# Performance work log

Measured on AMD Instinct MI355X. Metric: run time of the kernel, lower is better.

## Reference

```python
import jax, jax.numpy as jnp
from jax import lax
import numpy as np

NUM_HEADS = 8
K_RATIO = 0.5
GN_EPS = 1e-6
CLAMP = 32.0          # fp32 branch of the torch code
FILL = -1e9           # fp32 masked-fill value
L2_EPS = 1e-12        # torch F.normalize eps


def setup_inputs() -> dict:
    key = jax.random.key(0)
    k1, k2, k3 = jax.random.split(key, 3)
    B, C, H, W = 1, 256, 64, 64
    x = jax.random.normal(k1, (B, C, H, W), dtype=jnp.float32)
    w_qkv = jax.random.normal(k2, (3 * C, C), dtype=jnp.float32) * 0.02  # 1x1 conv, no bias
    w_proj = jax.random.normal(k3, (C, C), dtype=jnp.float32) * 0.02     # 1x1 conv, no bias
    gamma = jnp.ones((C,), dtype=jnp.float32)   # GroupNorm affine
    beta = jnp.zeros((C,), dtype=jnp.float32)
    return {"x": x, "w_qkv": w_qkv, "w_proj": w_proj, "gamma": gamma, "beta": beta}


def _l2norm(t):
    n = jnp.sqrt(jnp.sum(t * t, axis=-1, keepdims=True))
    return t / jnp.maximum(n, L2_EPS)


def reference(x, w_qkv, w_proj, gamma, beta):
    B, C, H, W = x.shape
    N = H * W
    hd = C // NUM_HEADS
    scale = hd ** -0.5

    # qkv 1x1 conv -> [B, 3C, H, W] -> [B, 3, heads, hd, N]
    qkv = jnp.einsum('bchw,oc->bohw', x, w_qkv).reshape(B, 3, NUM_HEADS, hd, N)
    q = jnp.swapaxes(qkv[:, 0], -1, -2)  # [B, heads, N, hd]
    k = jnp.swapaxes(qkv[:, 1], -1, -2)
    v = jnp.swapaxes(qkv[:, 2], -1, -2)

    q = _l2norm(q)
    k = _l2norm(k)

    attn = jnp.einsum('bhnd,bhmd->bhnm', q, k) * scale  # [B, heads, N, N]
    attn = jnp.clip(attn, -CLAMP, CLAMP)

    k_num = max(int(N * K_RATIO), 1)
    if k_num < N:
        # keep only top-k per row; threshold at the k-th largest value
        # (equivalent to torch.topk + scatter mask for continuous-valued scores)
        kth = lax.top_k(attn, k_num)[0][..., -1:]
        attn = jnp.where(attn >= kth, attn, FILL)

    attn = jax.nn.softmax(attn, axis=-1)
    out = jnp.einsum('bhnm,bhmd->bhnd', attn, v)          # [B, heads, N, hd]
    out = jnp.swapaxes(out, -1, -2).reshape(B, C, H, W)   # transpose(2,3) + reshape

    out = jnp.einsum('bchw,oc->bohw', out, w_proj)        # proj 1x1 conv

    # GroupNorm(groups=min(32, C//4)=32, eps=1e-6) with affine
    G = min(32, C // 4)
    xg = out.reshape(B, G, -1)
    mean = jnp.mean(xg, axis=-1, keepdims=True)
    var = jnp.var(xg, axis=-1, keepdims=True)
    xg = (xg - mean) / jnp.sqrt(var + GN_EPS)
    out = xg.reshape(B, C, H, W) * gamma[None, :, None, None] + beta[None, :, None, None]
    return out
```

## Files before the change

kernel.cpp:

```cpp
#include <hip/hip_runtime.h>


#define NTOK 4096
#define HD 32
#define NHEADS 8
#define KSEL 2048
#define SCALE 0.17677669529663689f
#define LOG2C 7.73937f


__device__ __forceinline__ unsigned fkey(float f) {
  unsigned b = __float_as_uint(f);
  return (b & 0x80000000u) ? ~b : (b | 0x80000000u);
}
__device__ __forceinline__ float unfkey(unsigned k) {
  unsigned b = (k & 0x80000000u) ? (k ^ 0x80000000u) : ~k;
  return __uint_as_float(b);
}
__device__ __forceinline__ unsigned rfl_u(unsigned x) {
  return __builtin_amdgcn_readfirstlane(x);
}
__device__ __forceinline__ unsigned probe_rf(unsigned klo, unsigned khi,
                                             float xlo, float xhi,
                                             int clo, int chi) {
  float t = xlo + (xhi - xlo) * ((float)(clo - KSEL) / (float)(clo - chi));
  unsigned k = fkey(t);
  if (k <= klo) k = klo + 1u;
  if (k > khi) k = khi;
  return k;
}


template <bool SCATTER>
__global__ __launch_bounds__(256) void gemm_k256(
    const float* __restrict__ A, const float* __restrict__ B,
    float* __restrict__ C0, float* __restrict__ C1, float* __restrict__ C2) {
  __shared__ float Wt[64][17];
  __shared__ float Xt[16][64];

  const int tid = threadIdx.x;
  const int tx = tid & 15, ty = tid >> 4;
  const int o0 = blockIdx.y * 64, n0 = blockIdx.x * 64;

  const int wr = tid >> 2, wc = (tid & 3) << 2;
  const int xr = tid >> 4, xc = (tid & 15) << 2;

  float4 acc[4];
#pragma unroll
  for (int i = 0; i < 4; ++i) acc[i] = make_float4(0.f, 0.f, 0.f, 0.f);

  for (int k0 = 0; k0 < 256; k0 += 16) {
    float4 wv = *(const float4*)(A + (o0 + wr) * 256 + k0 + wc);
    float4 xv = *(const float4*)(B + (k0 + xr) * 4096 + n0 + xc);
    Wt[wr][wc + 0] = wv.x; Wt[wr][wc + 1] = wv.y;
    Wt[wr][wc + 2] = wv.z; Wt[wr][wc + 3] = wv.w;
    *(float4*)&Xt[xr][xc] = xv;
    __syncthreads();
#pragma unroll
    for (int kk = 0; kk < 16; ++kk) {
      float4 b = *(const float4*)&Xt[kk][tx << 2];
#pragma unroll
      for (int i = 0; i < 4; ++i) {
        float a = Wt[(ty << 2) + i][kk];
        acc[i].x += a * b.x; acc[i].y += a * b.y;
        acc[i].z += a * b.z; acc[i].w += a * b.w;
      }
    }
    __syncthreads();
  }

  if (SCATTER) {
#pragma unroll
    for (int i = 0; i < 4; ++i) {
      int o = o0 + (ty << 2) + i;
      int which = o >> 8, rem = o & 255;
      int h = rem >> 5, d = rem & 31;
      int n = n0 + (tx << 2);
      if (which == 1) {
        *(float4*)(C1 + h * (HD * NTOK) + d * NTOK + n) = acc[i];
      } else {
        float* dst = (which == 0) ? C0 : C2;
        int base = h * (NTOK * HD) + d;
        dst[base + (n + 0) * HD] = acc[i].x;
        dst[base + (n + 1) * HD] = acc[i].y;
        dst[base + (n + 2) * HD] = acc[i].z;
        dst[base + (n + 3) * HD] = acc[i].w;
      }
    }
  } else {
#pragma unroll
    for (int i = 0; i < 4; ++i) {
      int o = o0 + (ty << 2) + i;
      *(float4*)(C0 + o * 4096 + n0 + (tx << 2)) = acc[i];
    }
  }
}


__global__ __launch_bounds__(256) void l2norm_q(float* __restrict__ Q) {
  const int tid = threadIdx.x;
  const int p = blockIdx.x * 8 + (tid >> 5);
  const int d = tid & 31;
  const int idx = p * HD + d;
  float v = Q[idx];
  float ss = v * v;
#pragma unroll
  for (int m = 16; m >= 1; m >>= 1) ss += __shfl_xor(ss, m, 32);
  float nrm = sqrtf(ss);
  Q[idx] = v * SCALE / fmaxf(nrm, 1e-12f);
}


__global__ __launch_bounds__(256) void l2norm_kt(float* __restrict__ KT) {
  const int n = blockIdx.x * 256 + threadIdx.x;
  float* P = KT + blockIdx.y * (HD * NTOK) + n;
  float v[HD];
  float ss = 0.f;
#pragma unroll
  for (int d = 0; d < HD; ++d) {
    v[d] = P[d * NTOK];
    ss += v[d] * v[d];
  }
  float inv = 1.f / fmaxf(sqrtf(ss), 1e-12f);
#pragma unroll
  for (int d = 0; d < HD; ++d) P[d * NTOK] = v[d] * inv;
}


__global__ __launch_bounds__(256, 5) void attn_kernel(
    const float* __restrict__ Q, const float* __restrict__ KT,
    const float* __restrict__ V, float* __restrict__ AO) {
  __shared__ __align__(16) unsigned char wtsT[NTOK][4];
  __shared__ float qs[128];
  __shared__ float pvred[4 * 8 * 4 * 4];
  __shared__ unsigned ired[2][4][2];
  __shared__ unsigned dred[4][4];

  const int tid = threadIdx.x;
  const int wv = tid >> 6, lane = tid & 63;
  const int head = blockIdx.x & 7;
  const int n0 = (blockIdx.x >> 3) << 2;

  const float* Qh = Q + head * (NTOK * HD);
  const float* KTh = KT + head * (HD * NTOK);
  const float* Vh = V + head * (NTOK * HD);

  if (tid < 128) qs[tid] = Qh[n0 * HD + tid];
  __syncthreads();

  float kr[4][16];
#pragma unroll
  for (int r = 0; r < 4; ++r)
#pragma unroll
    for (int j = 0; j < 16; ++j) kr[r][j] = 0.f;

  const int cb = tid << 2;
  const float* kbase = KTh + cb;
#define QK8(r, q, a, b, j0)                                                  \
  kr[r][(j0) + 0] += (q) * (a).x; kr[r][(j0) + 1] += (q) * (a).y;            \
  kr[r][(j0) + 2] += (q) * (a).z; kr[r][(j0) + 3] += (q) * (a).w;            \
  kr[r][(j0) + 4] += (q) * (b).x; kr[r][(j0) + 5] += (q) * (b).y;            \
  kr[r][(j0) + 6] += (q) * (b).z; kr[r][(j0) + 7] += (q) * (b).w;
#pragma unroll 1
  for (int dg = 0; dg < 8; ++dg) {
#pragma unroll 1
    for (int dd = 0; dd < 4; ++dd) {
      const int d = (dg << 2) + dd;
      const float* kp = kbase + d * NTOK;
      const float4 a0 = *(const float4*)(kp);
      const float4 b0 = *(const float4*)(kp + 1024);
      const float4 a1 = *(const float4*)(kp + 2048);
      const float4 b1 = *(const float4*)(kp + 3072);
      const float q0 = qs[d];
      const float q1 = qs[HD + d];
      const float q2 = qs[2 * HD + d];
      const float q3 = qs[3 * HD + d];
      QK8(0, q0, a0, b0, 0) QK8(1, q1, a0, b0, 0)
      QK8(2, q2, a0, b0, 0) QK8(3, q3, a0, b0, 0)
      QK8(0, q0, a1, b1, 8) QK8(1, q1, a1, b1, 8)
      QK8(2, q2, a1, b1, 8) QK8(3, q3, a1, b1, 8)
    }
  }
#undef QK8

  unsigned klo0 = 0x417FFFFFu, khi0 = 0xBE800000u;
  unsigned klo1 = 0x417FFFFFu, khi1 = 0xBE800000u;
  unsigned klo2 = 0x417FFFFFu, khi2 = 0xBE800000u;
  unsigned klo3 = 0x417FFFFFu, khi3 = 0xBE800000u;
  float xlo0 = -0.25f, xhi0 = 0.25f, xlo1 = -0.25f, xhi1 = 0.25f;
  float xlo2 = -0.25f, xhi2 = 0.25f, xlo3 = -0.25f, xhi3 = 0.25f;
  int clo0 = NTOK, chi0 = 0, clo1 = NTOK, chi1 = 0;
  int clo2 = NTOK, chi2 = 0, clo3 = NTOK, chi3 = 0;
  bool dn0 = false, dn1 = false, dn2 = false, dn3 = false;
  int slot = 0;
#pragma unroll 1
  for (int it = 0; it < 40; ++it) {
    unsigned m0 = dn0 ? klo0
        : ((it < 8 && (khi0 - klo0) > 65536u)
               ? rfl_u(probe_rf(klo0, khi0, xlo0, xhi0, clo0, chi0))
               : klo0 + ((khi0 - klo0 + 1u) >> 1));
    unsigned m1 = dn1 ? klo1
        : ((it < 8 && (khi1 - klo1) > 65536u)
               ? rfl_u(probe_rf(klo1, khi1, xlo1, xhi1, clo1, chi1))
               : klo1 + ((khi1 - klo1 + 1u) >> 1));
    unsigned m2 = dn2 ? klo2
        : ((it < 8 && (khi2 - klo2) > 65536u)
               ? rfl_u(probe_rf(klo2, khi2, xlo2, xhi2, clo2, chi2))
               : klo2 + ((khi2 - klo2 + 1u) >> 1));
    unsigned m3 = dn3 ? klo3
        : ((it < 8 && (khi3 - klo3) > 65536u)
               ? rfl_u(probe_rf(klo3, khi3, xlo3, xhi3, clo3, chi3))
               : klo3 + ((khi3 - klo3 + 1u) >> 1));
    unsigned c0 = 0, c1 = 0, c2 = 0, c3 = 0;
    if (!dn0) {
      const float f0 = unfkey(m0);
#pragma unroll
      for (int j = 0; j < 16; ++j) c0 += __popcll(__ballot(kr[0][j] >= f0));
    }
    if (!dn1) {
      const float f1 = unfkey(m1);
#pragma unroll
      for (int j = 0; j < 16; ++j) c1 += __popcll(__ballot(kr[1][j] >= f1));
    }
    if (!dn2) {
      const float f2 = unfkey(m2);
#pragma unroll
      for (int j = 0; j < 16; ++j) c2 += __popcll(__ballot(kr[2][j] >= f2));
    }
    if (!dn3) {
      const float f3 = unfkey(m3);
#pragma unroll
      for (int j = 0; j < 16; ++j) c3 += __popcll(__ballot(kr[3][j] >= f3));
    }
    if (lane == 0) {
      ired[slot][wv][0] = c0 | (c1 << 16);
      ired[slot][wv][1] = c2 | (c3 << 16);
    }
    __syncthreads();
    unsigned a01 = rfl_u(ired[slot][0][0] + ired[slot][1][0] +
                         ired[slot][2][0] + ired[slot][3][0]);
    unsigned a23 = rfl_u(ired[slot][0][1] + ired[slot][1][1] +
                         ired[slot][2][1] + ired[slot][3][1]);
    slot ^= 1;
    int C0 = (int)(a01 & 0xFFFFu), C1 = (int)(a01 >> 16);
    int C2 = (int)(a23 & 0xFFFFu), C3 = (int)(a23 >> 16);
#define BUPD(C, klo, khi, xlo, xhi, clo, chi, dn, mk)                        \
    if (!dn) {                                                               \
      if (C == KSEL) { klo = mk; dn = true; }                                \
      else if (C > KSEL) { klo = mk; xlo = unfkey(mk); clo = C; }            \
      else { khi = mk - 1u; xhi = unfkey(mk); chi = C; }                     \
      if (klo >= khi) dn = true;                                             \
    }
    BUPD(C0, klo0, khi0, xlo0, xhi0, clo0, chi0, dn0, m0)
    BUPD(C1, klo1, khi1, xlo1, xhi1, clo1, chi1, dn1, m1)
    BUPD(C2, klo2, khi2, xlo2, xhi2, clo2, chi2, dn2, m2)
    BUPD(C3, klo3, khi3, xlo3, xhi3, clo3, chi3, dn3, m3)
#undef BUPD
    if (dn0 && dn1 && dn2 && dn3) break;
  }
  const float tf0 = unfkey(klo0), tf1 = unfkey(klo1);
  const float tf2 = unfkey(klo2), tf3 = unfkey(klo3);

  unsigned id0 = 0, id1 = 0, id2 = 0, id3 = 0;
#pragma unroll
  for (int g = 0; g < 4; ++g) {
    unsigned pk[4];
#pragma unroll
    for (int t = 0; t < 4; ++t) {
      const int j = (g << 2) + t;
      float s0 = kr[0][j], s1 = kr[1][j], s2 = kr[2][j], s3 = kr[3][j];
      unsigned u0 = (s0 >= tf0) ? (unsigned)rintf(exp2f(__builtin_fmaf(s0, 1.44269504f, LOG2C))) : 0u;
      unsigned u1 = (s1 >= tf1) ? (unsigned)rintf(exp2f(__builtin_fmaf(s1, 1.44269504f, LOG2C))) : 0u;
      unsigned u2 = (s2 >= tf2) ? (unsigned)rintf(exp2f(__builtin_fmaf(s2, 1.44269504f, LOG2C))) : 0u;
      unsigned u3 = (s3 >= tf3) ? (unsigned)rintf(exp2f(__builtin_fmaf(s3, 1.44269504f, LOG2C))) : 0u;
      id0 += u0; id1 += u1; id2 += u2; id3 += u3;
      pk[t] = u0 | (u1 << 8) | (u2 << 16) | (u3 << 24);
    }
    const int col = (g << 10) + cb;
    *(uint4*)&wtsT[col][0] = make_uint4(pk[0], pk[1], pk[2], pk[3]);
  }
#pragma unroll
  for (int s = 1; s < 64; s <<= 1) {
    id0 += __shfl_xor(id0, s); id1 += __shfl_xor(id1, s);
    id2 += __shfl_xor(id2, s); id3 += __shfl_xor(id3, s);
  }
  if (lane == 0) *(uint4*)&dred[wv][0] = make_uint4(id0, id1, id2, id3);
  __syncthreads();
  const float dnm0 = (float)(dred[0][0] + dred[1][0] + dred[2][0] + dred[3][0]);
  const float dnm1 = (float)(dred[0][1] + dred[1][1] + dred[2][1] + dred[3][1]);
  const float dnm2 = (float)(dred[0][2] + dred[1][2] + dred[2][2] + dred[3][2]);
  const float dnm3 = (float)(dred[0][3] + dred[1][3] + dred[2][3] + dred[3][3]);

  const int slot5 = lane & 7, mg = lane >> 3;
  const int mbase = wv << 10;
  float av[4][4];
#pragma unroll
  for (int r = 0; r < 4; ++r)
#pragma unroll
    for (int c = 0; c < 4; ++c) av[r][c] = 0.f;

#pragma unroll 4
  for (int ii = 0; ii < 128; ++ii) {
    const int m = mbase + (ii << 3) + mg;
    unsigned wq = *(const unsigned*)&wtsT[m][0];
    float4 v = *(const float4*)(Vh + m * HD + (slot5 << 2));
    float w0 = (float)(wq & 0xFFu);
    float w1 = (float)((wq >> 8) & 0xFFu);
    float w2 = (float)((wq >> 16) & 0xFFu);
    float w3 = (float)(wq >> 24);
    av[0][0] += w0 * v.x; av[0][1] += w0 * v.y; av[0][2] += w0 * v.z; av[0][3] += w0 * v.w;
    av[1][0] += w1 * v.x; av[1][1] += w1 * v.y; av[1][2] += w1 * v.z; av[1][3] += w1 * v.w;
    av[2][0] += w2 * v.x; av[2][1] += w2 * v.y; av[2][2] += w2 * v.z; av[2][3] += w2 * v.w;
    av[3][0] += w3 * v.x; av[3][1] += w3 * v.y; av[3][2] += w3 * v.z; av[3][3] += w3 * v.w;
  }
#pragma unroll
  for (int r = 0; r < 4; ++r)
#pragma unroll
    for (int c = 0; c < 4; ++c) {
      float x = av[r][c];
      x += __shfl_xor(x, 8); x += __shfl_xor(x, 16); x += __shfl_xor(x, 32);
      av[r][c] = x;
    }
  if (mg == 0) {
#pragma unroll
    for (int r = 0; r < 4; ++r)
#pragma unroll
      for (int c = 0; c < 4; ++c)
        pvred[(((wv << 3) + slot5) * 4 + r) * 4 + c] = av[r][c];
  }
  __syncthreads();

  if (tid < 128) {
    const int r = tid >> 5, d = tid & 31;
    const int sl = d >> 2, c = d & 3;
    float val = 0.f;
#pragma unroll
    for (int w = 0; w < 4; ++w) val += pvred[(((w << 3) + sl) * 4 + r) * 4 + c];
    float dn = (r == 0) ? dnm0 : (r == 1) ? dnm1 : (r == 2) ? dnm2 : dnm3;
    val /= dn;
    AO[(head * HD + d) * NTOK + n0 + r] = val;
  }
}


__global__ __launch_bounds__(256) void gn_stats(const float* __restrict__ O,
                                                float* __restrict__ ST) {
  const int g = blockIdx.x, tid = threadIdx.x;
  const float4* p4 = (const float4*)(O + g * 32768);
  float s = 0.f, ss = 0.f;
  for (int i = tid; i < 8192; i += 256) {
    float4 v = p4[i];
    s += (v.x + v.y) + (v.z + v.w);
    ss += (v.x * v.x + v.y * v.y) + (v.z * v.z + v.w * v.w);
  }
#pragma unroll
  for (int m = 1; m < 64; m <<= 1) {
    s += __shfl_xor(s, m);
    ss += __shfl_xor(ss, m);
  }
  __shared__ float rs[4], rss[4];
  if ((tid & 63) == 0) { rs[tid >> 6] = s; rss[tid >> 6] = ss; }
  __syncthreads();
  if (tid == 0) {
    float S = rs[0] + rs[1] + rs[2] + rs[3];
    float SS = rss[0] + rss[1] + rss[2] + rss[3];
    float mean = S * (1.f / 32768.f);
    float var = SS * (1.f / 32768.f) - mean * mean;
    ST[g * 2] = mean;
    ST[g * 2 + 1] = rsqrtf(var + 1e-6f);
  }
}


__global__ __launch_bounds__(256) void gn_apply(float* __restrict__ O,
                                                const float* __restrict__ ST,
                                                const float* __restrict__ gamma,
                                                const float* __restrict__ beta) {
  const int i4 = blockIdx.x * 256 + threadIdx.x;
  const int c = i4 >> 10, g = c >> 3;
  const float a = ST[g * 2 + 1] * gamma[c];
  const float b = beta[c] - ST[g * 2] * a;
  float4 v = *(float4*)(O + (i4 << 2));
  v.x = v.x * a + b; v.y = v.y * a + b; v.z = v.z * a + b; v.w = v.w * a + b;
  *(float4*)(O + (i4 << 2)) = v;
}


extern "C" void kernel_launch(void* const* d_in, const int* in_sizes, int n_in,
                              void* d_out, int out_size, void* d_ws,
                              size_t ws_size, hipStream_t stream) {
  const float* x = (const float*)d_in[0];
  const float* w_qkv = (const float*)d_in[1];
  const float* w_proj = (const float*)d_in[2];
  const float* gamma = (const float*)d_in[3];
  const float* beta = (const float*)d_in[4];
  float* out = (float*)d_out;

  float* Q = (float*)d_ws;
  float* KT = Q + 1048576;
  float* V = KT + 1048576;
  float* AO = V + 1048576;
  float* ST = AO + 1048576;

  gemm_k256<true><<<dim3(64, 12), 256, 0, stream>>>(w_qkv, x, Q, KT, V);
  l2norm_q<<<4096, 256, 0, stream>>>(Q);
  l2norm_kt<<<dim3(16, 8), 256, 0, stream>>>(KT);
  attn_kernel<<<8192, 256, 0, stream>>>(Q, KT, V, AO);
  gemm_k256<false><<<dim3(64, 4), 256, 0, stream>>>(w_proj, AO, out, nullptr, nullptr);
  gn_stats<<<32, 256, 0, stream>>>(out, ST);
  gn_apply<<<1024, 256, 0, stream>>>(out, ST, gamma, beta);
}
```

Before: 511.4 us.

## Compute attention PV product with fp16 MFMA using transposed half-precision V

The QKV GEMM now writes V transposed and in fp16, and the attention kernel stores its quantized softmax weights as fp16 rows in shared memory. The scalar FMA loop for the P·V product, with its shuffle reductions, is replaced by 16x16x16 fp16 MFMA instructions. This is meant to cut VALU work and halve V memory traffic in the PV phase. In exchange, 12 of the 16 A-rows are zero padding, so much of the matrix unit's work is wasted, shared memory use doubles, and V loses precision by going to fp16.

```diff
diff --git a/kernel.cpp b/kernel.cpp
--- a/kernel.cpp
+++ b/kernel.cpp
@@ -7,6 +7,9 @@
 #define KSEL 2048
 #define SCALE 0.17677669529663689f
 #define LOG2C 7.73937f
+
+typedef _Float16 f16x4 __attribute__((ext_vector_type(4)));
+typedef float f32x4v __attribute__((ext_vector_type(4)));
 
 
 __device__ __forceinline__ unsigned fkey(float f) {
@@ -78,13 +81,18 @@
       int n = n0 + (tx << 2);
       if (which == 1) {
         *(float4*)(C1 + h * (HD * NTOK) + d * NTOK + n) = acc[i];
+      } else if (which == 2) {
+        _Float16* vh = (_Float16*)C2;
+        f16x4 hv;
+        hv[0] = (_Float16)acc[i].x; hv[1] = (_Float16)acc[i].y;
+        hv[2] = (_Float16)acc[i].z; hv[3] = (_Float16)acc[i].w;
+        *(f16x4*)(vh + h * (HD * NTOK) + d * NTOK + n) = hv;
       } else {
-        float* dst = (which == 0) ? C0 : C2;
         int base = h * (NTOK * HD) + d;
-        dst[base + (n + 0) * HD] = acc[i].x;
-        dst[base + (n + 1) * HD] = acc[i].y;
-        dst[base + (n + 2) * HD] = acc[i].z;
-        dst[base + (n + 3) * HD] = acc[i].w;
+        C0[base + (n + 0) * HD] = acc[i].x;
+        C0[base + (n + 1) * HD] = acc[i].y;
+        C0[base + (n + 2) * HD] = acc[i].z;
+        C0[base + (n + 3) * HD] = acc[i].w;
       }
     }
   } else {
@@ -129,10 +137,10 @@
 
 __global__ __launch_bounds__(256, 5) void attn_kernel(
     const float* __restrict__ Q, const float* __restrict__ KT,
-    const float* __restrict__ V, float* __restrict__ AO) {
-  __shared__ __align__(16) unsigned char wtsT[NTOK][4];
+    const _Float16* __restrict__ VT, float* __restrict__ AO) {
+  __shared__ __align__(16) _Float16 wt2[4][NTOK];
   __shared__ float qs[128];
-  __shared__ float pvred[4 * 8 * 4 * 4];
+  __shared__ float pvred[4 * 4 * 32];
   __shared__ unsigned ired[2][4][2];
   __shared__ unsigned dred[4][4];
 
@@ -143,7 +151,7 @@
 
   const float* Qh = Q + head * (NTOK * HD);
   const float* KTh = KT + head * (HD * NTOK);
-  const float* Vh = V + head * (NTOK * HD);
+  const _Float16* VTh = VT + head * (HD * NTOK);
 
   if (tid < 128) qs[tid] = Qh[n0 * HD + tid];
   __syncthreads();
@@ -264,20 +272,25 @@
   unsigned id0 = 0, id1 = 0, id2 = 0, id3 = 0;
 #pragma unroll
   for (int g = 0; g < 4; ++g) {
-    unsigned pk[4];
+    f16x4 w0v, w1v, w2v, w3v;
 #pragma unroll
     for (int t = 0; t < 4; ++t) {
       const int j = (g << 2) + t;
       float s0 = kr[0][j], s1 = kr[1][j], s2 = kr[2][j], s3 = kr[3][j];
-      unsigned u0 = (s0 >= tf0) ? (unsigned)rintf(exp2f(__builtin_fmaf(s0, 1.44269504f, LOG2C))) : 0u;
-      unsigned u1 = (s1 >= tf1) ? (unsigned)rintf(exp2f(__builtin_fmaf(s1, 1.44269504f, LOG2C))) : 0u;
-      unsigned u2 = (s2 >= tf2) ? (unsigned)rintf(exp2f(__builtin_fmaf(s2, 1.44269504f, LOG2C))) : 0u;
-      unsigned u3 = (s3 >= tf3) ? (unsigned)rintf(exp2f(__builtin_fmaf(s3, 1.44269504f, LOG2C))) : 0u;
-      id0 += u0; id1 += u1; id2 += u2; id3 += u3;
-      pk[t] = u0 | (u1 << 8) | (u2 << 16) | (u3 << 24);
+      float u0 = (s0 >= tf0) ? rintf(exp2f(__builtin_fmaf(s0, 1.44269504f, LOG2C))) : 0.f;
+      float u1 = (s1 >= tf1) ? rintf(exp2f(__builtin_fmaf(s1, 1.44269504f, LOG2C))) : 0.f;
+      float u2 = (s2 >= tf2) ? rintf(exp2f(__builtin_fmaf(s2, 1.44269504f, LOG2C))) : 0.f;
+      float u3 = (s3 >= tf3) ? rintf(exp2f(__builtin_fmaf(s3, 1.44269504f, LOG2C))) : 0.f;
+      id0 += (unsigned)u0; id1 += (unsigned)u1;
+      id2 += (unsigned)u2; id3 += (unsigned)u3;
+      w0v[t] = (_Float16)u0; w1v[t] = (_Float16)u1;
+      w2v[t] = (_Float16)u2; w3v[t] = (_Float16)u3;
     }
     const int col = (g << 10) + cb;
-    *(uint4*)&wtsT[col][0] = make_uint4(pk[0], pk[1], pk[2], pk[3]);
+    *(f16x4*)&wt2[0][col] = w0v;
+    *(f16x4*)&wt2[1][col] = w1v;
+    *(f16x4*)&wt2[2][col] = w2v;
+    *(f16x4*)&wt2[3][col] = w3v;
   }
 #pragma unroll
   for (int s = 1; s < 64; s <<= 1) {
@@ -291,51 +304,40 @@
   const float dnm2 = (float)(dred[0][2] + dred[1][2] + dred[2][2] + dred[3][2]);
   const float dnm3 = (float)(dred[0][3] + dred[1][3] + dred[2][3] + dred[3][3]);
 
-  const int slot5 = lane & 7, mg = lane >> 3;
-  const int mbase = wv << 10;
-  float av[4][4];
-#pragma unroll
-  for (int r = 0; r < 4; ++r)
-#pragma unroll
-    for (int c = 0; c < 4; ++c) av[r][c] = 0.f;
-
+  {
+    const int arow = lane & 15;
+    const int kgrp = lane >> 4;
+    const int koff = kgrp << 2;
+    const bool alive = arow < 4;
+    const _Float16* vb0 = VTh + arow * NTOK;
+    const _Float16* vb1 = VTh + (16 + arow) * NTOK;
+    const int mbase = wv << 10;
+    f32x4v acc0 = {0.f, 0.f, 0.f, 0.f}, acc1 = {0.f, 0.f, 0.f, 0.f};
 #pragma unroll 4
-  for (int ii = 0; ii < 128; ++ii) {
-    const int m = mbase + (ii << 3) + mg;
-    unsigned wq = *(const unsigned*)&wtsT[m][0];
-    float4 v = *(const float4*)(Vh + m * HD + (slot5 << 2));
-    float w0 = (float)(wq & 0xFFu);
-    float w1 = (float)((wq >> 8) & 0xFFu);
-    float w2 = (float)((wq >> 16) & 0xFFu);
-    float w3 = (float)(wq >> 24);
-    av[0][0] += w0 * v.x; av[0][1] += w0 * v.y; av[0][2] += w0 * v.z; av[0][3] += w0 * v.w;
-    av[1][0] += w1 * v.x; av[1][1] += w1 * v.y; av[1][2] += w1 * v.z; av[1][3] += w1 * v.w;
-    av[2][0] += w2 * v.x; av[2][1] += w2 * v.y; av[2][2] += w2 * v.z; av[2][3] += w2 * v.w;
-    av[3][0] += w3 * v.x; av[3][1] += w3 * v.y; av[3][2] += w3 * v.z; av[3][3] += w3 * v.w;
-  }
-#pragma unroll
-  for (int r = 0; r < 4; ++r)
-#pragma unroll
-    for (int c = 0; c < 4; ++c) {
-      float x = av[r][c];
-      x += __shfl_xor(x, 8); x += __shfl_xor(x, 16); x += __shfl_xor(x, 32);
-      av[r][c] = x;
-    }
-  if (mg == 0) {
-#pragma unroll
-    for (int r = 0; r < 4; ++r)
-#pragma unroll
-      for (int c = 0; c < 4; ++c)
-        pvred[(((wv << 3) + slot5) * 4 + r) * 4 + c] = av[r][c];
+    for (int s = 0; s < 64; ++s) {
+      const int k0 = mbase + (s << 4) + koff;
+      f16x4 a = {0, 0, 0, 0};
+      if (alive) a = *(const f16x4*)&wt2[arow][k0];
+      const f16x4 b0 = *(const f16x4*)(vb0 + k0);
+      const f16x4 b1 = *(const f16x4*)(vb1 + k0);
+      acc0 = __builtin_amdgcn_mfma_f32_16x16x16f16(a, b0, acc0, 0, 0, 0);
+      acc1 = __builtin_amdgcn_mfma_f32_16x16x16f16(a, b1, acc1, 0, 0, 0);
+    }
+    if (kgrp == 0) {
+#pragma unroll
+      for (int j = 0; j < 4; ++j) {
+        pvred[((wv << 2) + j) * 32 + arow] = acc0[j];
+        pvred[((wv << 2) + j) * 32 + 16 + arow] = acc1[j];
+      }
+    }
   }
   __syncthreads();
 
   if (tid < 128) {
     const int r = tid >> 5, d = tid & 31;
-    const int sl = d >> 2, c = d & 3;
     float val = 0.f;
 #pragma unroll
-    for (int w = 0; w < 4; ++w) val += pvred[(((w << 3) + sl) * 4 + r) * 4 + c];
+    for (int w = 0; w < 4; ++w) val += pvred[((w << 2) + r) * 32 + d];
     float dn = (r == 0) ? dnm0 : (r == 1) ? dnm1 : (r == 2) ? dnm2 : dnm3;
     val /= dn;
     AO[(head * HD + d) * NTOK + n0 + r] = val;
@@ -398,14 +400,14 @@
 
   float* Q = (float*)d_ws;
   float* KT = Q + 1048576;
-  float* V = KT + 1048576;
-  float* AO = V + 1048576;
+  float* VTr = KT + 1048576;
+  float* AO = VTr + 1048576;
   float* ST = AO + 1048576;
 
-  gemm_k256<true><<<dim3(64, 12), 256, 0, stream>>>(w_qkv, x, Q, KT, V);
+  gemm_k256<true><<<dim3(64, 12), 256, 0, stream>>>(w_qkv, x, Q, KT, VTr);
   l2norm_q<<<4096, 256, 0, stream>>>(Q);
   l2norm_kt<<<dim3(16, 8), 256, 0, stream>>>(KT);
-  attn_kernel<<<8192, 256, 0, stream>>>(Q, KT, V, AO);
+  attn_kernel<<<8192, 256, 0, stream>>>(Q, KT, (const _Float16*)VTr, AO);
   gemm_k256<false><<<dim3(64, 4), 256, 0, stream>>>(w_proj, AO, out, nullptr, nullptr);
   gn_stats<<<32, 256, 0, stream>>>(out, ST);
   gn_apply<<<1024, 256, 0, stream>>>(out, ST, gamma, beta);
```

Result: slower. 743.6 us (+45.4%).

## Pack normalized K into fp16 pairs and compute QK scores with fdot2

Applied to the files above, without the earlier changes.

The K normalization kernel now writes K as packed fp16 pairs, and the attention kernel packs Q into fp16 pairs in shared memory. It then computes the QK scores with v_dot2 fp16 instructions accumulating in fp32. This halves K load bandwidth and instruction count in the score loop. The risk is that fp16 rounding of Q and K perturbs the scores, which can change top-k threshold selection near ties and cost accuracy.

```diff
diff --git a/kernel.cpp b/kernel.cpp
--- a/kernel.cpp
+++ b/kernel.cpp
@@ -8,6 +8,11 @@
 #define SCALE 0.17677669529663689f
 #define LOG2C 7.73937f
 
+typedef __fp16 f16x2 __attribute__((ext_vector_type(2)));
+
+#define USE_DOT2 (__has_builtin(__builtin_amdgcn_fdot2) && \
+                  __has_builtin(__builtin_amdgcn_cvt_pkrtz))
+
 
 __device__ __forceinline__ unsigned fkey(float f) {
   unsigned b = __float_as_uint(f);
@@ -19,6 +24,12 @@
 }
 __device__ __forceinline__ unsigned rfl_u(unsigned x) {
   return __builtin_amdgcn_readfirstlane(x);
+}
+__device__ __forceinline__ f16x2 asv2h(unsigned u) {
+  union { unsigned u; f16x2 h; } c; c.u = u; return c.h;
+}
+__device__ __forceinline__ unsigned asu32(f16x2 h) {
+  union { f16x2 h; unsigned u; } c; c.h = h; return c.u;
 }
 __device__ __forceinline__ unsigned probe_rf(unsigned klo, unsigned khi,
                                              float xlo, float xhi,
@@ -111,7 +122,7 @@
 }
 
 
-__global__ __launch_bounds__(256) void l2norm_kt(float* __restrict__ KT) {
+__global__ __launch_bounds__(256) void l2norm_kt_pack(float* __restrict__ KT) {
   const int n = blockIdx.x * 256 + threadIdx.x;
   float* P = KT + blockIdx.y * (HD * NTOK) + n;
   float v[HD];
@@ -122,8 +133,17 @@
     ss += v[d] * v[d];
   }
   float inv = 1.f / fmaxf(sqrtf(ss), 1e-12f);
-#pragma unroll
-  for (int d = 0; d < HD; ++d) P[d * NTOK] = v[d] * inv;
+  unsigned* O = (unsigned*)P;
+#pragma unroll
+  for (int d2 = 0; d2 < 16; ++d2) {
+#if USE_DOT2
+    O[d2 * NTOK] = asu32(
+        __builtin_amdgcn_cvt_pkrtz(v[2 * d2] * inv, v[2 * d2 + 1] * inv));
+#else
+    f16x2 p; p[0] = (__fp16)(v[2 * d2] * inv); p[1] = (__fp16)(v[2 * d2 + 1] * inv);
+    O[d2 * NTOK] = asu32(p);
+#endif
+  }
 }
 
 
@@ -132,6 +152,7 @@
     const float* __restrict__ V, float* __restrict__ AO) {
   __shared__ __align__(16) unsigned char wtsT[NTOK][4];
   __shared__ float qs[128];
+  __shared__ unsigned qs2u[4][16];
   __shared__ float pvred[4 * 8 * 4 * 4];
   __shared__ unsigned ired[2][4][2];
   __shared__ unsigned dred[4][4];
@@ -147,6 +168,18 @@
 
   if (tid < 128) qs[tid] = Qh[n0 * HD + tid];
   __syncthreads();
+  if (tid < 64) {
+    const int r = tid >> 4, d2 = tid & 15;
+#if USE_DOT2
+    qs2u[r][d2] = asu32(__builtin_amdgcn_cvt_pkrtz(
+        qs[r * HD + (d2 << 1)], qs[r * HD + (d2 << 1) + 1]));
+#else
+    f16x2 p; p[0] = (__fp16)qs[r * HD + (d2 << 1)];
+    p[1] = (__fp16)qs[r * HD + (d2 << 1) + 1];
+    qs2u[r][d2] = asu32(p);
+#endif
+  }
+  __syncthreads();
 
   float kr[4][16];
 #pragma unroll
@@ -155,33 +188,56 @@
     for (int j = 0; j < 16; ++j) kr[r][j] = 0.f;
 
   const int cb = tid << 2;
-  const float* kbase = KTh + cb;
-#define QK8(r, q, a, b, j0)                                                  \
-  kr[r][(j0) + 0] += (q) * (a).x; kr[r][(j0) + 1] += (q) * (a).y;            \
-  kr[r][(j0) + 2] += (q) * (a).z; kr[r][(j0) + 3] += (q) * (a).w;            \
-  kr[r][(j0) + 4] += (q) * (b).x; kr[r][(j0) + 5] += (q) * (b).y;            \
-  kr[r][(j0) + 6] += (q) * (b).z; kr[r][(j0) + 7] += (q) * (b).w;
+  const unsigned* k16 = (const unsigned*)KTh + cb;
 #pragma unroll 1
-  for (int dg = 0; dg < 8; ++dg) {
-#pragma unroll 1
-    for (int dd = 0; dd < 4; ++dd) {
-      const int d = (dg << 2) + dd;
-      const float* kp = kbase + d * NTOK;
-      const float4 a0 = *(const float4*)(kp);
-      const float4 b0 = *(const float4*)(kp + 1024);
-      const float4 a1 = *(const float4*)(kp + 2048);
-      const float4 b1 = *(const float4*)(kp + 3072);
-      const float q0 = qs[d];
-      const float q1 = qs[HD + d];
-      const float q2 = qs[2 * HD + d];
-      const float q3 = qs[3 * HD + d];
-      QK8(0, q0, a0, b0, 0) QK8(1, q1, a0, b0, 0)
-      QK8(2, q2, a0, b0, 0) QK8(3, q3, a0, b0, 0)
-      QK8(0, q0, a1, b1, 8) QK8(1, q1, a1, b1, 8)
-      QK8(2, q2, a1, b1, 8) QK8(3, q3, a1, b1, 8)
-    }
-  }
-#undef QK8
+  for (int d2 = 0; d2 < 16; ++d2) {
+    const unsigned* kp = k16 + d2 * NTOK;
+    const uint4 kv0 = *(const uint4*)(kp);
+    const uint4 kv1 = *(const uint4*)(kp + 1024);
+    const uint4 kv2 = *(const uint4*)(kp + 2048);
+    const uint4 kv3 = *(const uint4*)(kp + 3072);
+    const unsigned qu0 = qs2u[0][d2], qu1 = qs2u[1][d2];
+    const unsigned qu2 = qs2u[2][d2], qu3 = qs2u[3][d2];
+#if USE_DOT2
+    const f16x2 q0 = asv2h(qu0), q1 = asv2h(qu1);
+    const f16x2 q2 = asv2h(qu2), q3 = asv2h(qu3);
+#define DOT16(r, qv)                                                         \
+    kr[r][0]  = __builtin_amdgcn_fdot2(qv, asv2h(kv0.x), kr[r][0],  false);  \
+    kr[r][1]  = __builtin_amdgcn_fdot2(qv, asv2h(kv0.y), kr[r][1],  false);  \
+    kr[r][2]  = __builtin_amdgcn_fdot2(qv, asv2h(kv0.z), kr[r][2],  false);  \
+    kr[r][3]  = __builtin_amdgcn_fdot2(qv, asv2h(kv0.w), kr[r][3],  false);  \
+    kr[r][4]  = __builtin_amdgcn_fdot2(qv, asv2h(kv1.x), kr[r][4],  false);  \
+    kr[r][5]  = __builtin_amdgcn_fdot2(qv, asv2h(kv1.y), kr[r][5],  false);  \
+    kr[r][6]  = __builtin_amdgcn_fdot2(qv, asv2h(kv1.z), kr[r][6],  false);  \
+    kr[r][7]  = __builtin_amdgcn_fdot2(qv, asv2h(kv1.w), kr[r][7],  false);  \
+    kr[r][8]  = __builtin_amdgcn_fdot2(qv, asv2h(kv2.x), kr[r][8],  false);  \
+    kr[r][9]  = __builtin_amdgcn_fdot2(qv, asv2h(kv2.y), kr[r][9],  false);  \
+    kr[r][10] = __builtin_amdgcn_fdot2(qv, asv2h(kv2.z), kr[r][10], false);  \
+    kr[r][11] = __builtin_amdgcn_fdot2(qv, asv2h(kv2.w), kr[r][11], false);  \
+    kr[r][12] = __builtin_amdgcn_fdot2(qv, asv2h(kv3.x), kr[r][12], false);  \
+    kr[r][13] = __builtin_amdgcn_fdot2(qv, asv2h(kv3.y), kr[r][13], false);  \
+    kr[r][14] = __builtin_amdgcn_fdot2(qv, asv2h(kv3.z), kr[r][14], false);  \
+    kr[r][15] = __builtin_amdgcn_fdot2(qv, asv2h(kv3.w), kr[r][15], false);
+    DOT16(0, q0) DOT16(1, q1) DOT16(2, q2) DOT16(3, q3)
+#undef DOT16
+#else
+#define DOTF(r, qu)                                                          \
+    {                                                                        \
+      const f16x2 qq = asv2h(qu);                                            \
+      const float qa = (float)qq[0], qb = (float)qq[1];                      \
+      const unsigned kk[16] = {kv0.x, kv0.y, kv0.z, kv0.w, kv1.x, kv1.y,     \
+                               kv1.z, kv1.w, kv2.x, kv2.y, kv2.z, kv2.w,     \
+                               kv3.x, kv3.y, kv3.z, kv3.w};                  \
+      _Pragma("unroll")                                                      \
+      for (int j = 0; j < 16; ++j) {                                         \
+        const f16x2 kh = asv2h(kk[j]);                                       \
+        kr[r][j] += qa * (float)kh[0] + qb * (float)kh[1];                   \
+      }                                                                      \
+    }
+    DOTF(0, qu0) DOTF(1, qu1) DOTF(2, qu2) DOTF(3, qu3)
+#undef DOTF
+#endif
+  }
 
   unsigned klo0 = 0x417FFFFFu, khi0 = 0xBE800000u;
   unsigned klo1 = 0x417FFFFFu, khi1 = 0xBE800000u;
@@ -404,7 +460,7 @@
 
   gemm_k256<true><<<dim3(64, 12), 256, 0, stream>>>(w_qkv, x, Q, KT, V);
   l2norm_q<<<4096, 256, 0, stream>>>(Q);
-  l2norm_kt<<<dim3(16, 8), 256, 0, stream>>>(KT);
+  l2norm_kt_pack<<<dim3(16, 8), 256, 0, stream>>>(KT);
   attn_kernel<<<8192, 256, 0, stream>>>(Q, KT, V, AO);
   gemm_k256<false><<<dim3(64, 4), 256, 0, stream>>>(w_proj, AO, out, nullptr, nullptr);
   gn_stats<<<32, 256, 0, stream>>>(out, ST);
```

Result: faster. 452.8 us (-11.5%).
